# Kernel tuning notes

Measured on AMD Instinct MI355X. Metric: run time of the kernel, lower is better.

Reference implementation:

```python
import jax, jax.numpy as jnp
import numpy as np
import math

EPS = 0.1
MAX_ITERS = 50
C_CLAMP = 1.0e6


def _cost_matrix(x, y):
    # Squared Euclidean cost ||x_i - y_j||^2 via GEMM expansion.
    x2 = jnp.sum(x * x, axis=1)[:, None]   # (n,1)
    y2 = jnp.sum(y * y, axis=1)[None, :]   # (1,m)
    C = x2 + y2 - 2.0 * (x @ y.T)          # (n,m)
    return jnp.clip(C, 0.0, C_CLAMP)


def _ot_cost(x, y):
    n, m = x.shape[0], y.shape[0]
    C = _cost_matrix(x, y)
    log_mu = -math.log(n)  # uniform weights (scalar, broadcasts)
    log_nu = -math.log(m)
    f0 = jnp.zeros((n,), dtype=x.dtype)
    g0 = jnp.zeros((m,), dtype=x.dtype)

    def step(carry, _):
        f, g = carry
        f = -EPS * jax.nn.logsumexp((g[None, :] - C) / EPS + log_nu, axis=1)
        g = -EPS * jax.nn.logsumexp((f[:, None] - C) / EPS + log_mu, axis=0)
        return (f, g), None

    (f, g), _ = jax.lax.scan(step, (f0, g0), None, length=MAX_ITERS)
    mu = jnp.exp(jnp.asarray(log_mu, dtype=x.dtype))
    nu = jnp.exp(jnp.asarray(log_nu, dtype=x.dtype))
    return jnp.sum(f) * mu + jnp.sum(g) * nu


def setup_inputs() -> dict:
    key = jax.random.key(0)
    kx, ky = jax.random.split(key)
    x = jax.random.normal(kx, (4096, 512), dtype=jnp.float32)
    y = jax.random.normal(ky, (4096, 512), dtype=jnp.float32)
    return {"x": x, "y": y}


def reference(x, y):
    ot_xy = _ot_cost(x, y)
    ot_xx = _ot_cost(x, x)
    ot_yy = _ot_cost(y, y)
    return jax.nn.relu(ot_xy - 0.5 * ot_xx - 0.5 * ot_yy)
```

## Files before the change

kernel.cpp:

```cpp
#include <hip/hip_runtime.h>
#include <hip/hip_bf16.h>
#include <math.h>

#define N 4096
#define D 512
#define SINK_PASSES 100

#define K_LOG2 14.426950408889634f
#define TWO_K  28.853900817779268f
#define NEG_EPS_LN2 (-0.06931471805599453f)
#define EPS_NEG_LOGMU 0.8317766166719343f

#define CAP 512
#define MARGIN 600.0f

typedef __bf16   bf16x8 __attribute__((ext_vector_type(8)));
typedef _Float16 halfx8 __attribute__((ext_vector_type(8)));
typedef float    floatx4 __attribute__((ext_vector_type(4)));
typedef unsigned short ushortx8v __attribute__((ext_vector_type(8)));

__global__ void cvt_bf16_kernel(const float* __restrict__ in, __bf16* __restrict__ out, int count) {
    int idx = blockIdx.x * blockDim.x + threadIdx.x;
    if (idx < count) out[idx] = (__bf16)in[idx];
}

__global__ void sqnorm_kernel(const float* __restrict__ in, float* __restrict__ out) {
    int row = blockIdx.x;
    const float* p = in + (size_t)row * D;
    float s = 0.f;
    for (int k = threadIdx.x; k < D; k += 64) { float v = p[k]; s += v * v; }
    for (int off = 32; off > 0; off >>= 1) s += __shfl_down(s, off);
    if (threadIdx.x == 0) out[row] = s;
}

__global__ __launch_bounds__(256) void gemm128_kernel(
    const __bf16* __restrict__ A, const __bf16* __restrict__ Bm,
    _Float16* __restrict__ out1, _Float16* __restrict__ out2, int sym) {
    if (sym && blockIdx.x > blockIdx.y) return;
    __shared__ char smem[34816];
    __bf16* ldsA = (__bf16*)smem;
    __bf16* ldsB = ldsA + 128 * 64;

    int t = threadIdx.x;
    int w = t >> 6, lane = t & 63;
    int m = lane & 15, q = lane >> 4;
    int wr = w & 1, wc = w >> 1;
    int m0 = blockIdx.x * 128, n0 = blockIdx.y * 128;

    int srow = t >> 1, shalf = t & 1;
    const bf16x8* gA = (const bf16x8*)(A  + (size_t)(m0 + srow) * D + shalf * 32);
    const bf16x8* gB = (const bf16x8*)(Bm + (size_t)(n0 + srow) * D + shalf * 32);

    floatx4 acc[4][4];
#pragma unroll
    for (int i = 0; i < 4; i++)
#pragma unroll
        for (int j = 0; j < 4; j++) acc[i][j] = (floatx4){0.f, 0.f, 0.f, 0.f};

    for (int slab = 0; slab < 8; slab++) {
        bf16x8 va[4], vb[4];
#pragma unroll
        for (int i = 0; i < 4; i++) {
            va[i] = gA[slab * 8 + i];
            vb[i] = gB[slab * 8 + i];
        }
        __syncthreads();
#pragma unroll
        for (int i = 0; i < 4; i++) {
            int cp = (shalf * 4 + i) ^ (srow & 7);
            *(bf16x8*)(ldsA + srow * 64 + cp * 8) = va[i];
            *(bf16x8*)(ldsB + srow * 64 + cp * 8) = vb[i];
        }
        __syncthreads();
#pragma unroll
        for (int kk = 0; kk < 2; kk++) {
            bf16x8 af[4], bfr[4];
#pragma unroll
            for (int mt = 0; mt < 4; mt++) {
                int cp = (kk * 4 + q) ^ (m & 7);
                af[mt]  = *(const bf16x8*)(ldsA + (wr * 64 + mt * 16 + m) * 64 + cp * 8);
                bfr[mt] = *(const bf16x8*)(ldsB + (wc * 64 + mt * 16 + m) * 64 + cp * 8);
            }
#pragma unroll
            for (int mt = 0; mt < 4; mt++)
#pragma unroll
                for (int nt = 0; nt < 4; nt++)
                    acc[mt][nt] = __builtin_amdgcn_mfma_f32_16x16x32_bf16(
                        af[mt], bfr[nt], acc[mt][nt], 0, 0, 0);
        }
    }

    __syncthreads();
    _Float16* et = (_Float16*)smem + w * (64 * 66);
#pragma unroll
    for (int mt = 0; mt < 4; mt++)
#pragma unroll
        for (int nt = 0; nt < 4; nt++)
#pragma unroll
            for (int r = 0; r < 4; r++)
                et[(mt * 16 + q * 4 + r) * 66 + nt * 16 + m] = (_Float16)acc[mt][nt][r];

    int l3 = lane >> 3, c8 = lane & 7;
#pragma unroll
    for (int rr = 0; rr < 8; rr++) {
        int rl = rr * 8 + l3;
        halfx8 v = *(const halfx8*)(et + rl * 66 + c8 * 8);
        *(halfx8*)(out1 + (size_t)(m0 + wr * 64 + rl) * N + n0 + wc * 64 + c8 * 8) = v;
    }
#pragma unroll
    for (int rr = 0; rr < 8; rr++) {
        int rT = rr * 8 + l3;
        halfx8 v;
#pragma unroll
        for (int k = 0; k < 8; k++) v[k] = et[(c8 * 8 + k) * 66 + rT];
        *(halfx8*)(out2 + (size_t)(n0 + wc * 64 + rT) * N + m0 + wr * 64 + c8 * 8) = v;
    }
}

template<int BUILD>
__global__ __launch_bounds__(256) void lse_full3_kernel(
    const _Float16* __restrict__ Sxy, const _Float16* __restrict__ STxy,
    const _Float16* __restrict__ Sxx, const _Float16* __restrict__ Syy,
    const float* __restrict__ x2, const float* __restrict__ y2,
    float* __restrict__ Pxy0, float* __restrict__ Pxy1,
    float* __restrict__ Pxx0, float* __restrict__ Pxx1,
    float* __restrict__ Pyy0, float* __restrict__ Pyy1,
    int odd,
    unsigned int* __restrict__ cand, int* __restrict__ cnt,
    float* __restrict__ prevmax) {
    __shared__ float gykT[8 * 512];
    int pair = blockIdx.x >> 10;
    int blk = blockIdx.x & 1023;
    const _Float16* M;
    const float *own, *other, *pin;
    float* pout;
    if (pair == 0) {
        if (odd) { M = Sxy;  own = x2; other = y2; pin = Pxy0; pout = Pxy1; }
        else     { M = STxy; own = y2; other = x2; pin = Pxy1; pout = Pxy0; }
    } else if (pair == 1) {
        M = Sxx; own = x2; other = x2;
        if (odd) { pin = Pxx0; pout = Pxx1; } else { pin = Pxx1; pout = Pxx0; }
    } else {
        M = Syy; own = y2; other = y2;
        if (odd) { pin = Pyy0; pout = Pyy1; } else { pin = Pyy1; pout = Pyy0; }
    }

    int wave = threadIdx.x >> 6, lane = threadIdx.x & 63;

    {
        const floatx4* pi4 = (const floatx4*)pin;
        const floatx4* so4 = (const floatx4*)other;
        for (int tt = threadIdx.x; tt < N / 4; tt += 256) {
            floatx4 p = pi4[tt], o = so4[tt];
            int j = tt * 4;
#pragma unroll
            for (int k2 = 0; k2 < 4; k2++) {
                int jj = j + k2;
                gykT[(jj & 7) * 512 + (jj >> 3)] = (p[k2] - o[k2]) * K_LOG2;
            }
        }
    }
    __syncthreads();

    int row = blk * 4 + wave;
    int set = pair * 2 + (odd ? 0 : 1);
    int idx = set * N + row;
    float thr = 0.f;
    size_t cbase = 0;
    int ncand = 0;
    unsigned long long lt_mask = (1ull << lane) - 1ull;
    if (BUILD) { thr = prevmax[idx] - MARGIN; cbase = (size_t)idx * CAP; }

    const halfx8* srow = (const halfx8*)(M + (size_t)row * N);
    float m = -INFINITY, s = 0.f;
#pragma unroll
    for (int c = 0; c < 8; c++) {
        int chunk = c * 64 + lane;
        halfx8 sv = srow[chunk];
        int j0 = chunk * 8;
        float u[8];
#pragma unroll
        for (int k = 0; k < 8; k++)
            u[k] = fmaf((float)sv[k], TWO_K, gykT[k * 512 + chunk]);
        float mloc = fmaxf(fmaxf(fmaxf(u[0], u[1]), fmaxf(u[2], u[3])),
                           fmaxf(fmaxf(u[4], u[5]), fmaxf(u[6], u[7])));
        if (BUILD) {
            if (__ballot(mloc >= thr)) {
                ushortx8v sb = __builtin_bit_cast(ushortx8v, sv);
#pragma unroll
                for (int k = 0; k < 8; k++) {
                    bool hit = (u[k] >= thr);
                    unsigned long long mask = __ballot(hit);
                    if (hit) {
                        int slot = ncand + __popcll(mask & lt_mask);
                        if (slot < CAP)
                            cand[cbase + slot] = ((unsigned int)(j0 + k) << 16) | (unsigned int)sb[k];
                    }
                    ncand += (int)__popcll(mask);
                }
            }
        }
        float M2 = fmaxf(m, mloc);
        float acc = 0.f;
#pragma unroll
        for (int k = 0; k < 8; k++) acc += exp2f(u[k] - M2);
        s = s * exp2f(m - M2) + acc;
        m = M2;
    }
    for (int off = 32; off > 0; off >>= 1) {
        float m2 = __shfl_down(m, off), s2 = __shfl_down(s, off);
        float Mx = fmaxf(m, m2);
        s = s * exp2f(m - Mx) + s2 * exp2f(m2 - Mx);
        m = Mx;
    }
    if (lane == 0) {
        float xk = own[row] * K_LOG2;
        pout[row] = NEG_EPS_LN2 * (m + __log2f(s) - xk) + EPS_NEG_LOGMU;
        prevmax[idx] = m;
        if (BUILD) cnt[idx] = ncand;
    }
}

__global__ __launch_bounds__(256) void lse_sparse3_kernel(
    const _Float16* __restrict__ Sxy, const _Float16* __restrict__ STxy,
    const _Float16* __restrict__ Sxx, const _Float16* __restrict__ Syy,
    const float* __restrict__ x2, const float* __restrict__ y2,
    float* __restrict__ Pxy0, float* __restrict__ Pxy1,
    float* __restrict__ Pxx0, float* __restrict__ Pxx1,
    float* __restrict__ Pyy0, float* __restrict__ Pyy1,
    int odd,
    const unsigned int* __restrict__ cand, const int* __restrict__ cnt,
    float* __restrict__ prevmax) {
    int wave = threadIdx.x >> 6, lane = threadIdx.x & 63;
    int gwave = blockIdx.x * 4 + wave;
    int pair = gwave >> 10;
    int pwave = gwave & 1023;
    const _Float16* M;
    const float *own, *other, *pin;
    float* pout;
    if (pair == 0) {
        if (odd) { M = Sxy;  own = x2; other = y2; pin = Pxy0; pout = Pxy1; }
        else     { M = STxy; own = y2; other = x2; pin = Pxy1; pout = Pxy0; }
    } else if (pair == 1) {
        M = Sxx; own = x2; other = x2;
        if (odd) { pin = Pxx0; pout = Pxx1; } else { pin = Pxx1; pout = Pxx0; }
    } else {
        M = Syy; own = y2; other = y2;
        if (odd) { pin = Pyy0; pout = Pyy1; } else { pin = Pyy1; pout = Pyy0; }
    }
    int set = pair * 2 + (odd ? 0 : 1);

    for (int i = 0; i < 4; i++) {
        int row = pwave * 4 + i;
        int idx = set * N + row;
        int c = cnt[idx];
        float m, s;
        if (c >= 1 && c <= CAP) {
            size_t cbase = (size_t)idx * CAP;
            int nb = (c + 63) >> 6;
            float uu[8];
            float lm = -INFINITY;
#pragma unroll 8
            for (int b = 0; b < 8; b++) {
                uu[b] = -INFINITY;
                if (b < nb) {
                    int t = b * 64 + lane;
                    if (t < c) {
                        unsigned int pk = cand[cbase + t];
                        int j = pk >> 16;
                        _Float16 h = __builtin_bit_cast(_Float16, (unsigned short)(pk & 0xffffu));
                        uu[b] = fmaf((float)h, TWO_K, (pin[j] - other[j]) * K_LOG2);
                    }
                    lm = fmaxf(lm, uu[b]);
                }
            }
            for (int off = 32; off > 0; off >>= 1)
                lm = fmaxf(lm, __shfl_xor(lm, off));
            float ls = 0.f;
#pragma unroll 8
            for (int b = 0; b < 8; b++)
                if (b < nb) ls += exp2f(uu[b] - lm);
            for (int off = 32; off > 0; off >>= 1)
                ls += __shfl_xor(ls, off);
            m = lm; s = ls;
        } else {
            m = -INFINITY; s = 0.f;
            const halfx8* rowp = (const halfx8*)(M + (size_t)row * N);
            for (int ch = lane; ch < N / 8; ch += 64) {
                halfx8 sv = rowp[ch];
                int j0 = ch * 8;
                floatx4 p0 = *(const floatx4*)(pin + j0);
                floatx4 p1 = *(const floatx4*)(pin + j0 + 4);
                floatx4 o0 = *(const floatx4*)(other + j0);
                floatx4 o1 = *(const floatx4*)(other + j0 + 4);
                float u[8];
#pragma unroll
                for (int k = 0; k < 4; k++) {
                    u[k]     = fmaf((float)sv[k],     TWO_K, (p0[k] - o0[k]) * K_LOG2);
                    u[k + 4] = fmaf((float)sv[k + 4], TWO_K, (p1[k] - o1[k]) * K_LOG2);
                }
                float mloc = fmaxf(fmaxf(fmaxf(u[0], u[1]), fmaxf(u[2], u[3])),
                                   fmaxf(fmaxf(u[4], u[5]), fmaxf(u[6], u[7])));
                float M2 = fmaxf(m, mloc);
                float acc = 0.f;
#pragma unroll
                for (int k = 0; k < 8; k++) acc += exp2f(u[k] - M2);
                s = s * exp2f(m - M2) + acc;
                m = M2;
            }
            for (int off = 32; off > 0; off >>= 1) {
                float m2 = __shfl_xor(m, off), s2 = __shfl_xor(s, off);
                float Mx = fmaxf(m, m2);
                float a1 = (m  == -INFINITY) ? 0.f : s  * exp2f(m  - Mx);
                float a2 = (m2 == -INFINITY) ? 0.f : s2 * exp2f(m2 - Mx);
                m = Mx; s = a1 + a2;
            }
        }
        if (lane == 0) {
            float xk = own[row] * K_LOG2;
            pout[row] = NEG_EPS_LN2 * (m + __log2f(s) - xk) + EPS_NEG_LOGMU;
            prevmax[idx] = m;
        }
    }
}

__global__ void finalize_kernel(const float* __restrict__ fxy, const float* __restrict__ gxy,
                                const float* __restrict__ fxx, const float* __restrict__ gxx,
                                const float* __restrict__ fyy, const float* __restrict__ gyy,
                                float* __restrict__ out) {
    __shared__ float sb[256];
    float s = 0.f;
    for (int t = threadIdx.x; t < N; t += 256)
        s += (fxy[t] + gxy[t]) - 0.5f * (fxx[t] + gxx[t]) - 0.5f * (fyy[t] + gyy[t]);
    sb[threadIdx.x] = s;
    __syncthreads();
    for (int off = 128; off > 0; off >>= 1) {
        if (threadIdx.x < off) sb[threadIdx.x] += sb[threadIdx.x + off];
        __syncthreads();
    }
    if (threadIdx.x == 0) {
        float v = sb[0] * (1.0f / 4096.0f);
        out[0] = v > 0.f ? v : 0.f;
    }
}

extern "C" void kernel_launch(void* const* d_in, const int* in_sizes, int n_in,
                              void* d_out, int out_size, void* d_ws, size_t ws_size,
                              hipStream_t stream) {
    const float* x = (const float*)d_in[0];
    const float* y = (const float*)d_in[1];

    const size_t SZ_S = (size_t)N * N * sizeof(_Float16);
    const size_t SZ_B = (size_t)N * D * sizeof(__bf16);
    const size_t SZ_CAND = (size_t)6 * N * CAP * sizeof(unsigned int);

    char* w = (char*)d_ws;
    _Float16* Sxy  = (_Float16*)w; w += SZ_S;
    _Float16* STxy = (_Float16*)w; w += SZ_S;
    _Float16* Sxx  = (_Float16*)w; w += SZ_S;
    _Float16* Syy  = (_Float16*)w; w += SZ_S;
    __bf16* xb = (__bf16*)w;       w += SZ_B;
    __bf16* yb = (__bf16*)w;       w += SZ_B;
    unsigned int* cand = (unsigned int*)w; w += SZ_CAND;
    int* cnt = (int*)w;            w += (size_t)6 * N * sizeof(int);
    float* prevmax = (float*)w;    w += (size_t)6 * N * sizeof(float);
    float* x2 = (float*)w;         w += N * sizeof(float);
    float* y2 = (float*)w;         w += N * sizeof(float);
    float* P[6];
    for (int i = 0; i < 6; i++) { P[i] = (float*)w; w += N * sizeof(float); }

    const size_t need = (size_t)(w - (char*)d_ws);
    const bool sparse_ok = (ws_size >= need);

    cvt_bf16_kernel<<<(N * D + 255) / 256, 256, 0, stream>>>(x, xb, N * D);
    cvt_bf16_kernel<<<(N * D + 255) / 256, 256, 0, stream>>>(y, yb, N * D);
    sqnorm_kernel<<<N, 64, 0, stream>>>(x, x2);
    sqnorm_kernel<<<N, 64, 0, stream>>>(y, y2);

    gemm128_kernel<<<dim3(32, 32), 256, 0, stream>>>(xb, yb, Sxy, STxy, 0);
    gemm128_kernel<<<dim3(32, 32), 256, 0, stream>>>(xb, xb, Sxx, Sxx, 1);
    gemm128_kernel<<<dim3(32, 32), 256, 0, stream>>>(yb, yb, Syy, Syy, 1);

    hipMemsetAsync(P[0], 0, N * sizeof(float), stream);
    hipMemsetAsync(P[2], 0, N * sizeof(float), stream);
    hipMemsetAsync(P[4], 0, N * sizeof(float), stream);

    for (int p = 1; p <= SINK_PASSES; p++) {
        int odd = p & 1;
        bool build = sparse_ok && (p == 9 || p == 10 || p == 49 || p == 50);
        bool full  = !sparse_ok || p <= 8 || build;

        if (full) {
            if (build)
                lse_full3_kernel<1><<<3 * (N / 4), 256, 0, stream>>>(
                    Sxy, STxy, Sxx, Syy, x2, y2,
                    P[0], P[1], P[2], P[3], P[4], P[5], odd, cand, cnt, prevmax);
            else
                lse_full3_kernel<0><<<3 * (N / 4), 256, 0, stream>>>(
                    Sxy, STxy, Sxx, Syy, x2, y2,
                    P[0], P[1], P[2], P[3], P[4], P[5], odd, cand, cnt, prevmax);
        } else {
            lse_sparse3_kernel<<<768, 256, 0, stream>>>(
                Sxy, STxy, Sxx, Syy, x2, y2,
                P[0], P[1], P[2], P[3], P[4], P[5], odd, cand, cnt, prevmax);
        }
    }
    finalize_kernel<<<1, 256, 0, stream>>>(P[1], P[0], P[3], P[2], P[5], P[4],
                                           (float*)d_out);
}
```

Measured before the change: 1.217 ms.

## Replace per-pass sparse LSE launches with persistent kernel using grid barrier

Moves the sparse Sinkhorn passes (11-48 and 51-100) into one persistent kernel of 192 blocks per segment. Blocks synchronise between passes with an atomic grid-wide barrier instead of separate kernel launches, and the final reduction is folded into the last persistent launch. It also fuses the bf16 conversion and squared-norm prep into one kernel, and merges the memsets into one. Half-wave rows use an online running-max LSE over candidates. This targets launch overhead across dozens of small passes, at the cost of lower parallelism (192 blocks) and a spin barrier that deadlocks if the blocks are not all resident at once.

```diff
diff --git a/kernel.cpp b/kernel.cpp
--- a/kernel.cpp
+++ b/kernel.cpp
@@ -4,7 +4,6 @@
 
 #define N 4096
 #define D 512
-#define SINK_PASSES 100
 
 #define K_LOG2 14.426950408889634f
 #define TWO_K  28.853900817779268f
@@ -13,24 +12,34 @@
 
 #define CAP 512
 #define MARGIN 600.0f
+#define PBLOCKS 192
 
 typedef __bf16   bf16x8 __attribute__((ext_vector_type(8)));
 typedef _Float16 halfx8 __attribute__((ext_vector_type(8)));
 typedef float    floatx4 __attribute__((ext_vector_type(4)));
 typedef unsigned short ushortx8v __attribute__((ext_vector_type(8)));
 
-__global__ void cvt_bf16_kernel(const float* __restrict__ in, __bf16* __restrict__ out, int count) {
-    int idx = blockIdx.x * blockDim.x + threadIdx.x;
-    if (idx < count) out[idx] = (__bf16)in[idx];
-}
-
-__global__ void sqnorm_kernel(const float* __restrict__ in, float* __restrict__ out) {
-    int row = blockIdx.x;
-    const float* p = in + (size_t)row * D;
-    float s = 0.f;
-    for (int k = threadIdx.x; k < D; k += 64) { float v = p[k]; s += v * v; }
-    for (int off = 32; off > 0; off >>= 1) s += __shfl_down(s, off);
-    if (threadIdx.x == 0) out[row] = s;
+__global__ __launch_bounds__(256) void prep_kernel(
+    const float* __restrict__ x, const float* __restrict__ y,
+    __bf16* __restrict__ xb, __bf16* __restrict__ yb,
+    float* __restrict__ x2, float* __restrict__ y2) {
+    int wave = threadIdx.x >> 6, lane = threadIdx.x & 63;
+    int r = blockIdx.x * 4 + wave;
+    const float* src = (r < N) ? x + (size_t)r * D : y + (size_t)(r - N) * D;
+    __bf16* dst      = (r < N) ? xb + (size_t)r * D : yb + (size_t)(r - N) * D;
+    float* sq        = (r < N) ? x2 + r : y2 + (r - N);
+    floatx4 a = *(const floatx4*)(src + lane * 8);
+    floatx4 b = *(const floatx4*)(src + lane * 8 + 4);
+    bf16x8 v;
+    float acc = 0.f;
+#pragma unroll
+    for (int k = 0; k < 4; k++) {
+        v[k] = (__bf16)a[k]; v[4 + k] = (__bf16)b[k];
+        acc += a[k] * a[k] + b[k] * b[k];
+    }
+    *(bf16x8*)(dst + lane * 8) = v;
+    for (int off = 32; off > 0; off >>= 1) acc += __shfl_down(acc, off);
+    if (lane == 0) *sq = acc;
 }
 
 __global__ __launch_bounds__(256) void gemm128_kernel(
@@ -151,12 +160,12 @@
         const floatx4* pi4 = (const floatx4*)pin;
         const floatx4* so4 = (const floatx4*)other;
         for (int tt = threadIdx.x; tt < N / 4; tt += 256) {
-            floatx4 p = pi4[tt], o = so4[tt];
+            floatx4 pv = pi4[tt], ov = so4[tt];
             int j = tt * 4;
 #pragma unroll
             for (int k2 = 0; k2 < 4; k2++) {
                 int jj = j + k2;
-                gykT[(jj & 7) * 512 + (jj >> 3)] = (p[k2] - o[k2]) * K_LOG2;
+                gykT[(jj & 7) * 512 + (jj >> 3)] = (pv[k2] - ov[k2]) * K_LOG2;
             }
         }
     }
@@ -186,7 +195,7 @@
                            fmaxf(fmaxf(u[4], u[5]), fmaxf(u[6], u[7])));
         if (BUILD) {
             if (__ballot(mloc >= thr)) {
-                ushortx8v sb = __builtin_bit_cast(ushortx8v, sv);
+                ushortx8v s8 = __builtin_bit_cast(ushortx8v, sv);
 #pragma unroll
                 for (int k = 0; k < 8; k++) {
                     bool hit = (u[k] >= thr);
@@ -194,7 +203,7 @@
                     if (hit) {
                         int slot = ncand + __popcll(mask & lt_mask);
                         if (slot < CAP)
-                            cand[cbase + slot] = ((unsigned int)(j0 + k) << 16) | (unsigned int)sb[k];
+                            cand[cbase + slot] = ((unsigned int)(j0 + k) << 16) | (unsigned int)s8[k];
                     }
                     ncand += (int)__popcll(mask);
                 }
@@ -214,112 +223,133 @@
         m = Mx;
     }
     if (lane == 0) {
-        float xk = own[row] * K_LOG2;
-        pout[row] = NEG_EPS_LN2 * (m + __log2f(s) - xk) + EPS_NEG_LOGMU;
+        pout[row] = NEG_EPS_LN2 * (m + __log2f(s) - own[row] * K_LOG2) + EPS_NEG_LOGMU;
         prevmax[idx] = m;
         if (BUILD) cnt[idx] = ncand;
     }
 }
 
-__global__ __launch_bounds__(256) void lse_sparse3_kernel(
+__global__ __launch_bounds__(256) void sparse_persist_kernel(
     const _Float16* __restrict__ Sxy, const _Float16* __restrict__ STxy,
     const _Float16* __restrict__ Sxx, const _Float16* __restrict__ Syy,
     const float* __restrict__ x2, const float* __restrict__ y2,
-    float* __restrict__ Pxy0, float* __restrict__ Pxy1,
-    float* __restrict__ Pxx0, float* __restrict__ Pxx1,
-    float* __restrict__ Pyy0, float* __restrict__ Pyy1,
-    int odd,
+    float* __restrict__ P0, float* __restrict__ P1,
+    float* __restrict__ P2, float* __restrict__ P3,
+    float* __restrict__ P4, float* __restrict__ P5,
     const unsigned int* __restrict__ cand, const int* __restrict__ cnt,
-    float* __restrict__ prevmax) {
-    int wave = threadIdx.x >> 6, lane = threadIdx.x & 63;
-    int gwave = blockIdx.x * 4 + wave;
-    int pair = gwave >> 10;
-    int pwave = gwave & 1023;
-    const _Float16* M;
-    const float *own, *other, *pin;
-    float* pout;
-    if (pair == 0) {
-        if (odd) { M = Sxy;  own = x2; other = y2; pin = Pxy0; pout = Pxy1; }
-        else     { M = STxy; own = y2; other = x2; pin = Pxy1; pout = Pxy0; }
-    } else if (pair == 1) {
-        M = Sxx; own = x2; other = x2;
-        if (odd) { pin = Pxx0; pout = Pxx1; } else { pin = Pxx1; pout = Pxx0; }
-    } else {
-        M = Syy; own = y2; other = y2;
-        if (odd) { pin = Pyy0; pout = Pyy1; } else { pin = Pyy1; pout = Pyy0; }
-    }
-    int set = pair * 2 + (odd ? 0 : 1);
-
-    for (int i = 0; i < 4; i++) {
-        int row = pwave * 4 + i;
-        int idx = set * N + row;
-        int c = cnt[idx];
-        float m, s;
-        if (c >= 1 && c <= CAP) {
-            size_t cbase = (size_t)idx * CAP;
-            int nb = (c + 63) >> 6;
-            float uu[8];
-            float lm = -INFINITY;
-#pragma unroll 8
-            for (int b = 0; b < 8; b++) {
-                uu[b] = -INFINITY;
-                if (b < nb) {
-                    int t = b * 64 + lane;
+    float* __restrict__ prevmax,
+    int p0, int npass, int* __restrict__ bar, int do_final, float* __restrict__ out)
+{
+    __shared__ float sb[256];
+    const int pair = blockIdx.x >> 6;
+    const int pblk = blockIdx.x & 63;
+    const int wave = threadIdx.x >> 6, lane = threadIdx.x & 63;
+    const int half = lane >> 5, hl = lane & 31;
+
+    const float* sqa = (pair == 2) ? y2 : x2;
+    const float* sqb = (pair == 1) ? x2 : y2;
+    const _Float16* Mrow = (pair == 0) ? Sxy : (pair == 1 ? Sxx : Syy);
+    const _Float16* Mcol = (pair == 0) ? STxy : Mrow;
+    float* PA = (pair == 0) ? P0 : (pair == 1 ? P2 : P4);
+    float* PB = (pair == 0) ? P1 : (pair == 1 ? P3 : P5);
+
+    int bt = 0;
+    for (int pi = 0; pi < npass; pi++) {
+        int p = p0 + pi;
+        int odd = p & 1;
+        const _Float16* M  = odd ? Mrow : Mcol;
+        const float* own   = odd ? sqa : sqb;
+        const float* other = odd ? sqb : sqa;
+        const float* pin   = odd ? PA : PB;
+        float* pout        = odd ? PB : PA;
+        int set = pair * 2 + (odd ? 0 : 1);
+
+        for (int i = 0; i < 16; i += 2) {
+            int row = pblk * 64 + wave * 16 + i + half;
+            int idx = set * N + row;
+            int c = cnt[idx];
+            float m = -INFINITY, s = 0.f;
+            if (c >= 1 && c <= CAP) {
+                size_t cbase = (size_t)idx * CAP;
+                for (int b = 0; b * 32 < c; b++) {
+                    int t = b * 32 + hl;
                     if (t < c) {
                         unsigned int pk = cand[cbase + t];
                         int j = pk >> 16;
                         _Float16 h = __builtin_bit_cast(_Float16, (unsigned short)(pk & 0xffffu));
-                        uu[b] = fmaf((float)h, TWO_K, (pin[j] - other[j]) * K_LOG2);
+                        float u = fmaf((float)h, TWO_K, (pin[j] - other[j]) * K_LOG2);
+                        if (u <= m) {
+                            s += exp2f(u - m);
+                        } else {
+                            s = s * exp2f(m - u) + 1.f;
+                            m = u;
+                        }
                     }
-                    lm = fmaxf(lm, uu[b]);
                 }
-            }
-            for (int off = 32; off > 0; off >>= 1)
-                lm = fmaxf(lm, __shfl_xor(lm, off));
-            float ls = 0.f;
-#pragma unroll 8
-            for (int b = 0; b < 8; b++)
-                if (b < nb) ls += exp2f(uu[b] - lm);
-            for (int off = 32; off > 0; off >>= 1)
-                ls += __shfl_xor(ls, off);
-            m = lm; s = ls;
-        } else {
-            m = -INFINITY; s = 0.f;
-            const halfx8* rowp = (const halfx8*)(M + (size_t)row * N);
-            for (int ch = lane; ch < N / 8; ch += 64) {
-                halfx8 sv = rowp[ch];
-                int j0 = ch * 8;
-                floatx4 p0 = *(const floatx4*)(pin + j0);
-                floatx4 p1 = *(const floatx4*)(pin + j0 + 4);
-                floatx4 o0 = *(const floatx4*)(other + j0);
-                floatx4 o1 = *(const floatx4*)(other + j0 + 4);
-                float u[8];
-#pragma unroll
-                for (int k = 0; k < 4; k++) {
-                    u[k]     = fmaf((float)sv[k],     TWO_K, (p0[k] - o0[k]) * K_LOG2);
-                    u[k + 4] = fmaf((float)sv[k + 4], TWO_K, (p1[k] - o1[k]) * K_LOG2);
+            } else {
+                const halfx8* rowp = (const halfx8*)(M + (size_t)row * N);
+                for (int ch = hl; ch < N / 8; ch += 32) {
+                    halfx8 sv = rowp[ch];
+                    int j0 = ch * 8;
+                    floatx4 pp0 = *(const floatx4*)(pin + j0);
+                    floatx4 pp1 = *(const floatx4*)(pin + j0 + 4);
+                    floatx4 oo0 = *(const floatx4*)(other + j0);
+                    floatx4 oo1 = *(const floatx4*)(other + j0 + 4);
+                    float u[8];
+#pragma unroll
+                    for (int k = 0; k < 4; k++) {
+                        u[k]     = fmaf((float)sv[k],     TWO_K, (pp0[k] - oo0[k]) * K_LOG2);
+                        u[k + 4] = fmaf((float)sv[k + 4], TWO_K, (pp1[k] - oo1[k]) * K_LOG2);
+                    }
+                    float mloc = fmaxf(fmaxf(fmaxf(u[0], u[1]), fmaxf(u[2], u[3])),
+                                       fmaxf(fmaxf(u[4], u[5]), fmaxf(u[6], u[7])));
+                    float M2 = fmaxf(m, mloc);
+                    float acc = 0.f;
+#pragma unroll
+                    for (int k = 0; k < 8; k++) acc += exp2f(u[k] - M2);
+                    s = s * exp2f(m - M2) + acc;
+                    m = M2;
                 }
-                float mloc = fmaxf(fmaxf(fmaxf(u[0], u[1]), fmaxf(u[2], u[3])),
-                                   fmaxf(fmaxf(u[4], u[5]), fmaxf(u[6], u[7])));
-                float M2 = fmaxf(m, mloc);
-                float acc = 0.f;
-#pragma unroll
-                for (int k = 0; k < 8; k++) acc += exp2f(u[k] - M2);
-                s = s * exp2f(m - M2) + acc;
-                m = M2;
-            }
-            for (int off = 32; off > 0; off >>= 1) {
+            }
+            for (int off = 16; off > 0; off >>= 1) {
                 float m2 = __shfl_xor(m, off), s2 = __shfl_xor(s, off);
                 float Mx = fmaxf(m, m2);
                 float a1 = (m  == -INFINITY) ? 0.f : s  * exp2f(m  - Mx);
                 float a2 = (m2 == -INFINITY) ? 0.f : s2 * exp2f(m2 - Mx);
                 m = Mx; s = a1 + a2;
             }
-        }
-        if (lane == 0) {
-            float xk = own[row] * K_LOG2;
-            pout[row] = NEG_EPS_LN2 * (m + __log2f(s) - xk) + EPS_NEG_LOGMU;
-            prevmax[idx] = m;
+            if (hl == 0) {
+                pout[row] = NEG_EPS_LN2 * (m + __log2f(s) - own[row] * K_LOG2)
+                            + EPS_NEG_LOGMU;
+                prevmax[idx] = m;
+            }
+        }
+
+        __threadfence();
+        __syncthreads();
+        bt += PBLOCKS;
+        if (threadIdx.x == 0) {
+            __hip_atomic_fetch_add(bar, 1, __ATOMIC_RELEASE, __HIP_MEMORY_SCOPE_AGENT);
+            while (__hip_atomic_load(bar, __ATOMIC_ACQUIRE, __HIP_MEMORY_SCOPE_AGENT) < bt)
+                __builtin_amdgcn_s_sleep(1);
+            __threadfence();
+        }
+        __syncthreads();
+    }
+
+    if (do_final && blockIdx.x == 0) {
+        float s = 0.f;
+        for (int t = threadIdx.x; t < N; t += 256)
+            s += (P1[t] + P0[t]) - 0.5f * (P3[t] + P2[t]) - 0.5f * (P5[t] + P4[t]);
+        sb[threadIdx.x] = s;
+        __syncthreads();
+        for (int off = 128; off > 0; off >>= 1) {
+            if (threadIdx.x < off) sb[threadIdx.x] += sb[threadIdx.x + off];
+            __syncthreads();
+        }
+        if (threadIdx.x == 0) {
+            float v = sb[0] * (1.0f / 4096.0f);
+            out[0] = v > 0.f ? v : 0.f;
         }
     }
 }
@@ -361,50 +391,53 @@
     _Float16* Syy  = (_Float16*)w; w += SZ_S;
     __bf16* xb = (__bf16*)w;       w += SZ_B;
     __bf16* yb = (__bf16*)w;       w += SZ_B;
-    unsigned int* cand = (unsigned int*)w; w += SZ_CAND;
     int* cnt = (int*)w;            w += (size_t)6 * N * sizeof(int);
     float* prevmax = (float*)w;    w += (size_t)6 * N * sizeof(float);
     float* x2 = (float*)w;         w += N * sizeof(float);
     float* y2 = (float*)w;         w += N * sizeof(float);
     float* P[6];
     for (int i = 0; i < 6; i++) { P[i] = (float*)w; w += N * sizeof(float); }
+    int* bar = (int*)w;            w += 4 * sizeof(int);
+    unsigned int* cand = (unsigned int*)w; w += SZ_CAND;
 
     const size_t need = (size_t)(w - (char*)d_ws);
     const bool sparse_ok = (ws_size >= need);
 
-    cvt_bf16_kernel<<<(N * D + 255) / 256, 256, 0, stream>>>(x, xb, N * D);
-    cvt_bf16_kernel<<<(N * D + 255) / 256, 256, 0, stream>>>(y, yb, N * D);
-    sqnorm_kernel<<<N, 64, 0, stream>>>(x, x2);
-    sqnorm_kernel<<<N, 64, 0, stream>>>(y, y2);
+    prep_kernel<<<2048, 256, 0, stream>>>(x, y, xb, yb, x2, y2);
 
     gemm128_kernel<<<dim3(32, 32), 256, 0, stream>>>(xb, yb, Sxy, STxy, 0);
     gemm128_kernel<<<dim3(32, 32), 256, 0, stream>>>(xb, xb, Sxx, Sxx, 1);
     gemm128_kernel<<<dim3(32, 32), 256, 0, stream>>>(yb, yb, Syy, Syy, 1);
 
-    hipMemsetAsync(P[0], 0, N * sizeof(float), stream);
-    hipMemsetAsync(P[2], 0, N * sizeof(float), stream);
-    hipMemsetAsync(P[4], 0, N * sizeof(float), stream);
-
-    for (int p = 1; p <= SINK_PASSES; p++) {
-        int odd = p & 1;
-        bool build = sparse_ok && (p == 9 || p == 10 || p == 49 || p == 50);
-        bool full  = !sparse_ok || p <= 8 || build;
-
-        if (full) {
-            if (build)
-                lse_full3_kernel<1><<<3 * (N / 4), 256, 0, stream>>>(
-                    Sxy, STxy, Sxx, Syy, x2, y2,
-                    P[0], P[1], P[2], P[3], P[4], P[5], odd, cand, cnt, prevmax);
-            else
-                lse_full3_kernel<0><<<3 * (N / 4), 256, 0, stream>>>(
-                    Sxy, STxy, Sxx, Syy, x2, y2,
-                    P[0], P[1], P[2], P[3], P[4], P[5], odd, cand, cnt, prevmax);
-        } else {
-            lse_sparse3_kernel<<<768, 256, 0, stream>>>(
+    hipMemsetAsync(P[0], 0, (size_t)6 * N * sizeof(float) + 4 * sizeof(int), stream);
+
+    if (sparse_ok) {
+        for (int p = 1; p <= 8; p++)
+            lse_full3_kernel<0><<<3 * (N / 4), 256, 0, stream>>>(
                 Sxy, STxy, Sxx, Syy, x2, y2,
-                P[0], P[1], P[2], P[3], P[4], P[5], odd, cand, cnt, prevmax);
-        }
-    }
-    finalize_kernel<<<1, 256, 0, stream>>>(P[1], P[0], P[3], P[2], P[5], P[4],
-                                           (float*)d_out);
-}
+                P[0], P[1], P[2], P[3], P[4], P[5], p & 1, cand, cnt, prevmax);
+        for (int p = 9; p <= 10; p++)
+            lse_full3_kernel<1><<<3 * (N / 4), 256, 0, stream>>>(
+                Sxy, STxy, Sxx, Syy, x2, y2,
+                P[0], P[1], P[2], P[3], P[4], P[5], p & 1, cand, cnt, prevmax);
+        sparse_persist_kernel<<<PBLOCKS, 256, 0, stream>>>(
+            Sxy, STxy, Sxx, Syy, x2, y2,
+            P[0], P[1], P[2], P[3], P[4], P[5],
+            cand, cnt, prevmax, 11, 38, bar + 0, 0, (float*)d_out);
+        for (int p = 49; p <= 50; p++)
+            lse_full3_kernel<1><<<3 * (N / 4), 256, 0, stream>>>(
+                Sxy, STxy, Sxx, Syy, x2, y2,
+                P[0], P[1], P[2], P[3], P[4], P[5], p & 1, cand, cnt, prevmax);
+        sparse_persist_kernel<<<PBLOCKS, 256, 0, stream>>>(
+            Sxy, STxy, Sxx, Syy, x2, y2,
+            P[0], P[1], P[2], P[3], P[4], P[5],
+            cand, cnt, prevmax, 51, 50, bar + 1, 1, (float*)d_out);
+    } else {
+        for (int p = 1; p <= 100; p++)
+            lse_full3_kernel<0><<<3 * (N / 4), 256, 0, stream>>>(
+                Sxy, STxy, Sxx, Syy, x2, y2,
+                P[0], P[1], P[2], P[3], P[4], P[5], p & 1, cand, cnt, prevmax);
+        finalize_kernel<<<1, 256, 0, stream>>>(P[1], P[0], P[3], P[2], P[5], P[4],
+                                               (float*)d_out);
+    }
+}
```

After: 4.401 ms. +261.7%, slower.
